# Optimization experiments

Hardware: AMD Instinct MI355X
Metric: run time of the kernel (lower is better)

## Reference

```python
import jax, jax.numpy as jnp
import numpy as np

B, S, D, H = 2, 2048, 512, 8
DH = D // H  # depth per head = 64
MAX_SEQ = 2048


def setup_inputs() -> dict:
    key = jax.random.key(0)
    ks = jax.random.split(key, 12)
    sc = 1.0 / np.sqrt(D)
    inp = {
        "v": jax.random.normal(ks[0], (B, S, D), jnp.float32),
        "k": jax.random.normal(ks[1], (B, S, D), jnp.float32),
        "q": jax.random.normal(ks[2], (B, S, D), jnp.float32),
        # causal look-ahead mask: 1.0 where attention is disallowed (j > i)
        "mask": jnp.triu(jnp.ones((S, S), jnp.float32), k=1)[None, None, :, :],
        "Wq": jax.random.normal(ks[3], (D, D), jnp.float32) * sc,
        "bq": jnp.zeros((D,), jnp.float32),
        "Wk": jax.random.normal(ks[4], (D, D), jnp.float32) * sc,
        "bk": jnp.zeros((D,), jnp.float32),
        "Wv": jax.random.normal(ks[5], (D, D), jnp.float32) * sc,
        "bv": jnp.zeros((D,), jnp.float32),
        "Wo": jax.random.normal(ks[6], (D, D), jnp.float32) * sc,
        "bo": jnp.zeros((D,), jnp.float32),
        # relative position embedding table [max_seq, depth]
        "E": jax.random.normal(ks[7], (MAX_SEQ, DH), jnp.float32) * 0.02,
    }
    return inp


def reference(v, k, q, mask, Wq, bq, Wk, bk, Wv, bv, Wo, bo, E):
    b, s, d = q.shape
    split = lambda x: x.reshape(b, s, H, DH).transpose(0, 2, 1, 3)  # [b,h,s,dh]
    qh = split(q @ Wq + bq)
    kh = split(k @ Wk + bk)
    vh = split(v @ Wv + bv)

    # QK^T logits [b,h,lq,lk]
    logits = jnp.einsum("bhqd,bhkd->bhqk", qh, kh)

    # relative position bias (Music Transformer skewing trick)
    Eq = E[max(MAX_SEQ - s, 0):, :]          # left embedding slice [s, dh]
    m = Eq.shape[0]
    QE = jnp.einsum("bhld,md->bhlm", qh, Eq)  # [b,h,s,m]
    # keep entries where col >= m-1-row (qe masking)
    rows = jnp.arange(s)[:, None]
    cols = jnp.arange(m)[None, :]
    QE = QE * (cols >= (m - 1 - rows)).astype(QE.dtype)
    # skew: pad one zero column on the left, reshape, drop first row
    padded = jnp.pad(QE, ((0, 0), (0, 0), (0, 0), (1, 0)))  # [b,h,s,m+1]
    Srel = padded.reshape(b, H, m + 1, s)[:, :, 1:, :]       # [b,h,m,s]
    # here len_q == len_k == s, so Srel is [b,h,s,s] with no extra pad/slice

    logits = (logits + Srel) / jnp.sqrt(jnp.float32(DH))
    logits = logits + mask * -1e9
    attn = jax.nn.softmax(logits, axis=-1)
    out = jnp.einsum("bhqk,bhkd->bhqd", attn, vh)
    out = out.transpose(0, 2, 1, 3).reshape(b, s, d)
    return out @ Wo + bo, attn
```

## Files before the change

### kernel.cpp

```cpp
#include <hip/hip_runtime.h>

typedef __bf16 bf16x8 __attribute__((ext_vector_type(8)));
typedef float f32x4 __attribute__((ext_vector_type(4)));

#define MFMA(a, b, c) __builtin_amdgcn_mfma_f32_16x16x32_bf16((a), (b), (c), 0, 0, 0)

__global__ __launch_bounds__(256)
void prep_kernel(const float* __restrict__ Wq, const float* __restrict__ Wk,
                 const float* __restrict__ Wv, const float* __restrict__ Wo,
                 const float* __restrict__ E,
                 __bf16* __restrict__ WT, __bf16* __restrict__ Ebf)
{
    __shared__ float tl[32][33];
    const int bx = blockIdx.x, t = threadIdx.x;
    if (bx < 1024) {
        const int wi = bx >> 8, tile = bx & 255;
        const float* W = wi == 0 ? Wq : wi == 1 ? Wk : wi == 2 ? Wv : Wo;
        __bf16* dst = WT + (size_t)wi * 512 * 512;
        const int k0 = (tile >> 4) << 5, n0 = (tile & 15) << 5;
        const int tx = t & 31, ty = t >> 5;
        #pragma unroll
        for (int i = 0; i < 4; ++i) {
            int r = ty + i * 8;
            tl[r][tx] = W[(size_t)(k0 + r) * 512 + n0 + tx];
        }
        __syncthreads();
        #pragma unroll
        for (int i = 0; i < 4; ++i) {
            int r = ty + i * 8;
            dst[(size_t)(n0 + r) * 512 + k0 + tx] = (__bf16)tl[tx][r];
        }
    } else {
        int idx = (bx - 1024) * 256 + t;
        for (int i = idx; i < 2048 * 64; i += 8 * 256)
            Ebf[i] = (__bf16)E[i];
    }
}

__global__ __launch_bounds__(256, 3)
void proj_kernel(const float* __restrict__ xq, const float* __restrict__ xk,
                 const float* __restrict__ xv, const __bf16* __restrict__ WT,
                 const float* __restrict__ bq, const float* __restrict__ bk,
                 const float* __restrict__ bv,
                 __bf16* __restrict__ outQ, __bf16* __restrict__ outK,
                 __bf16* __restrict__ outV)
{
    __shared__ __bf16 As[128][72];
    __shared__ __bf16 Bs[64][72];
    const int t = threadIdx.x;
    const int z = blockIdx.y;
    const float* x = z == 0 ? xq : z == 1 ? xk : xv;
    const float* bias = z == 0 ? bq : z == 1 ? bk : bv;
    const __bf16* Wt = WT + (size_t)z * (512 * 512);
    __bf16* outp = z == 0 ? outQ : z == 1 ? outK : outV;

    const int bx = blockIdx.x;
    const int m0 = (bx >> 3) << 7;
    const int n0 = (bx & 7) << 6;
    const int w = t >> 6, lane = t & 63, quad = lane >> 4, l16 = lane & 15;

    const int ar = t >> 1, ac = (t & 1) << 5;
    const int br = t >> 2, bc = (t & 3) << 4;

    float4 xr[8];
    int4 wr0, wr1;
    {
        const float4* xs = (const float4*)(x + (size_t)(m0 + ar) * 512 + ac);
        #pragma unroll
        for (int j = 0; j < 8; ++j) xr[j] = xs[j];
        const int4* wsrc = (const int4*)(Wt + (size_t)(n0 + br) * 512 + bc);
        wr0 = wsrc[0]; wr1 = wsrc[1];
    }

    f32x4 acc[2][4];
    #pragma unroll
    for (int rb = 0; rb < 2; ++rb)
        #pragma unroll
        for (int nt = 0; nt < 4; ++nt) acc[rb][nt] = (f32x4)0.f;

    for (int k0 = 0; k0 < 512; k0 += 64) {
        __syncthreads();
        {
            __bf16 tb[32];
            #pragma unroll
            for (int j = 0; j < 8; ++j) {
                tb[j * 4 + 0] = (__bf16)xr[j].x;
                tb[j * 4 + 1] = (__bf16)xr[j].y;
                tb[j * 4 + 2] = (__bf16)xr[j].z;
                tb[j * 4 + 3] = (__bf16)xr[j].w;
            }
            *(int4*)&As[ar][ac]      = ((int4*)tb)[0];
            *(int4*)&As[ar][ac + 8]  = ((int4*)tb)[1];
            *(int4*)&As[ar][ac + 16] = ((int4*)tb)[2];
            *(int4*)&As[ar][ac + 24] = ((int4*)tb)[3];
            *(int4*)&Bs[br][bc]     = wr0;
            *(int4*)&Bs[br][bc + 8] = wr1;
        }
        __syncthreads();
        if (k0 + 64 < 512) {
            const float4* xs = (const float4*)(x + (size_t)(m0 + ar) * 512 + k0 + 64 + ac);
            #pragma unroll
            for (int j = 0; j < 8; ++j) xr[j] = xs[j];
            const int4* wsrc = (const int4*)(Wt + (size_t)(n0 + br) * 512 + k0 + 64 + bc);
            wr0 = wsrc[0]; wr1 = wsrc[1];
        }
        bf16x8 bf[8];
        #pragma unroll
        for (int nt = 0; nt < 4; ++nt) {
            bf[nt * 2]     = *(const bf16x8*)&Bs[nt * 16 + l16][quad * 8];
            bf[nt * 2 + 1] = *(const bf16x8*)&Bs[nt * 16 + l16][32 + quad * 8];
        }
        #pragma unroll
        for (int rb = 0; rb < 2; ++rb) {
            bf16x8 a0 = *(const bf16x8*)&As[w * 32 + rb * 16 + l16][quad * 8];
            bf16x8 a1 = *(const bf16x8*)&As[w * 32 + rb * 16 + l16][32 + quad * 8];
            #pragma unroll
            for (int nt = 0; nt < 4; ++nt) {
                acc[rb][nt] = MFMA(a0, bf[nt * 2], acc[rb][nt]);
                acc[rb][nt] = MFMA(a1, bf[nt * 2 + 1], acc[rb][nt]);
            }
        }
    }
    #pragma unroll
    for (int rb = 0; rb < 2; ++rb) {
        #pragma unroll
        for (int nt = 0; nt < 4; ++nt) {
            const int n = n0 + nt * 16 + l16;
            const float bb = bias[n];
            const int h = n >> 6, dh = n & 63;
            #pragma unroll
            for (int i = 0; i < 4; ++i) {
                const int m = m0 + w * 32 + rb * 16 + quad * 4 + i;
                const int b = m >> 11, s = m & 2047;
                outp[(((size_t)(b * 8 + h) * 2048 + s) << 6) + dh] = (__bf16)(acc[rb][nt][i] + bb);
            }
        }
    }
}

__global__ __launch_bounds__(256, 3)
void attn_kernel(const __bf16* __restrict__ Qh, const __bf16* __restrict__ Kh,
                 const __bf16* __restrict__ Vh, const __bf16* __restrict__ Eb,
                 __bf16* __restrict__ Pout, float* __restrict__ attn,
                 __bf16* __restrict__ ctx)
{
    __shared__ __bf16 SA[64][72];
    __shared__ __bf16 SB[64][72];
    __shared__ __bf16 SC[128][72];
    __shared__ float linv_s[64];

    const int t = threadIdx.x;
    const int bx = blockIdx.x;
    const int tt = bx & 31;
    const int bh = ((bx & 255) >> 5) + ((bx >> 8) << 3);
    const int q0 = (bx < 256 ? (31 - tt) : tt) << 6;
    const int w = t >> 6, lane = t & 63, quad = lane >> 4, l16 = lane & 15;
    const int qw = w << 4;

    const __bf16* Qg = Qh + (size_t)bh * (2048 * 64);
    const __bf16* Kg = Kh + (size_t)bh * (2048 * 64);
    const __bf16* Vg = Vh + (size_t)bh * (2048 * 64);
    __bf16* Pg = Pout + (size_t)bh * (2048 * 2048);
    float* attng = attn + (size_t)bh * (2048 * 2048);

    const int sr = t >> 2, sc = (t & 3) << 4;
    const int er = t >> 1, ec = (t & 1) << 5;

    {
        const int4* src = (const int4*)(Qg + (size_t)(q0 + sr) * 64 + sc);
        int4 v0 = src[0], v1 = src[1];
        *(int4*)&SA[sr][sc]     = v0;
        *(int4*)&SA[sr][sc + 8] = v1;
    }
    __syncthreads();
    const bf16x8 qa0 = *(const bf16x8*)&SA[qw + l16][quad * 8];
    const bf16x8 qa1 = *(const bf16x8*)&SA[qw + l16][32 + quad * 8];
    __syncthreads();

    __bf16 (* const Ps)[72] = SA;

    const int nkt = (q0 >> 6) + 1;
    const float csc = 0.125f * 1.44269504f;

    float lsum[4] = {0.f, 0.f, 0.f, 0.f};

    int4 kreg0, kreg1, ereg0, ereg1, ereg2, ereg3;
    {
        const int4* ks = (const int4*)(Kg + (size_t)sr * 64 + sc);
        kreg0 = ks[0]; kreg1 = ks[1];
        int e = 1984 - q0 + er; if (e > 2047) e = 2047;
        const int4* es = (const int4*)(Eb + (size_t)e * 64 + ec);
        ereg0 = es[0]; ereg1 = es[1]; ereg2 = es[2]; ereg3 = es[3];
    }

    for (int kt = 0; kt < nkt; ++kt) {
        const int k0 = kt << 6;
        if (kt > 0) {
            int4 p0 = *(const int4*)&Ps[sr][sc];
            int4 p1 = *(const int4*)&Ps[sr][sc + 8];
            __bf16* dst = Pg + (size_t)(q0 + sr) * 2048 + (k0 - 64) + sc;
            *(int4*)dst       = p0;
            *(int4*)(dst + 8) = p1;
        }
        *(int4*)&SB[sr][sc]     = kreg0;
        *(int4*)&SB[sr][sc + 8] = kreg1;
        *(int4*)&SC[er][ec]      = ereg0;
        *(int4*)&SC[er][ec + 8]  = ereg1;
        *(int4*)&SC[er][ec + 16] = ereg2;
        *(int4*)&SC[er][ec + 24] = ereg3;
        __syncthreads();

        if (kt + 1 < nkt) {
            const int k0n = (kt + 1) << 6;
            const int4* ks = (const int4*)(Kg + (size_t)(k0n + sr) * 64 + sc);
            kreg0 = ks[0]; kreg1 = ks[1];
            int e = 1984 - q0 + k0n + er; if (e > 2047) e = 2047;
            const int4* es = (const int4*)(Eb + (size_t)e * 64 + ec);
            ereg0 = es[0]; ereg1 = es[1]; ereg2 = es[2]; ereg3 = es[3];
        }

        f32x4 aqk[4];
        #pragma unroll
        for (int nt = 0; nt < 4; ++nt) {
            aqk[nt] = (f32x4)0.f;
            bf16x8 b0 = *(const bf16x8*)&SB[nt * 16 + l16][quad * 8];
            bf16x8 b1 = *(const bf16x8*)&SB[nt * 16 + l16][32 + quad * 8];
            aqk[nt] = MFMA(qa0, b0, aqk[nt]);
            aqk[nt] = MFMA(qa1, b1, aqk[nt]);
        }
        f32x4 aqe[5];
        #pragma unroll
        for (int jj = 0; jj < 5; ++jj) {
            aqe[jj] = (f32x4)0.f;
            const int ebr = 48 - qw + jj * 16 + l16;
            bf16x8 b0 = *(const bf16x8*)&SC[ebr][quad * 8];
            bf16x8 b1 = *(const bf16x8*)&SC[ebr][32 + quad * 8];
            aqe[jj] = MFMA(qa0, b0, aqe[jj]);
            aqe[jj] = MFMA(qa1, b1, aqe[jj]);
        }

        #pragma unroll
        for (int i = 0; i < 4; ++i) {
            const int d  = quad * 4 + i;
            const int ql = qw + d;
            const int qq = q0 + ql;
            const int sp = (l16 + 15 - d) & 15;
            const bool hi = l16 > d;
            #pragma unroll
            for (int nt = 0; nt < 4; ++nt) {
                float g0 = __shfl(aqe[nt][i], sp, 16);
                float g1 = __shfl(aqe[nt + 1][i], sp, 16);
                float qe = hi ? g1 : g0;
                float ev = (k0 + nt * 16 + l16 <= qq)
                         ? exp2f((aqk[nt][i] + qe) * csc) : 0.f;
                lsum[i] += ev;
                Ps[ql][nt * 16 + l16] = (__bf16)ev;
            }
        }
        __syncthreads();
    }
    {
        int4 p0 = *(const int4*)&Ps[sr][sc];
        int4 p1 = *(const int4*)&Ps[sr][sc + 8];
        __bf16* dst = Pg + (size_t)(q0 + sr) * 2048 + ((nkt - 1) << 6) + sc;
        *(int4*)dst       = p0;
        *(int4*)(dst + 8) = p1;
    }
    {
        #pragma unroll
        for (int i = 0; i < 4; ++i) {
            float v = lsum[i];
            #pragma unroll
            for (int m = 1; m < 16; m <<= 1) v += __shfl_xor(v, m, 16);
            if (l16 == 0) linv_s[qw + quad * 4 + i] = 1.0f / v;
        }
    }
    __syncthreads();

    const float li = linv_s[qw + l16];
    float linvr[4];
    #pragma unroll
    for (int i = 0; i < 4; ++i) linvr[i] = linv_s[qw + quad * 4 + i];

    f32x4 acc_o[4];
    #pragma unroll
    for (int i = 0; i < 4; ++i) acc_o[i] = (f32x4)0.f;

    int4 vreg0, vreg1;
    {
        const int4* vs = (const int4*)(Vg + (size_t)sr * 64 + sc);
        vreg0 = vs[0]; vreg1 = vs[1];
    }

    for (int kt = 0; kt < nkt; ++kt) {
        const int k0 = kt << 6;
        __syncthreads();
        {
            __bf16 tmp[16];
            *(int4*)&tmp[0] = vreg0; *(int4*)&tmp[8] = vreg1;
            #pragma unroll
            for (int j = 0; j < 16; ++j) {
                const int dh = sc + j;
                SB[dh][sr ^ (((dh >> 4) & 1) << 3)] = tmp[j];
            }
        }
        __syncthreads();
        if (kt + 1 < nkt) {
            const int4* vs = (const int4*)(Vg + (size_t)(((kt + 1) << 6) + sr) * 64 + sc);
            vreg0 = vs[0]; vreg1 = vs[1];
        }

        const __bf16* prow = Pg + (size_t)(q0 + qw + l16) * 2048 + k0 + quad * 8;
        int4 praw0 = *(const int4*)prow;
        int4 praw1 = *(const int4*)(prow + 32);
        bf16x8 pa0 = *(bf16x8*)&praw0;
        bf16x8 pa1 = *(bf16x8*)&praw1;

        #pragma unroll
        for (int dt = 0; dt < 4; ++dt) {
            const int xr = (dt & 1) << 3;
            bf16x8 vb0 = *(const bf16x8*)&SB[dt * 16 + l16][(quad * 8) ^ xr];
            bf16x8 vb1 = *(const bf16x8*)&SB[dt * 16 + l16][32 + ((quad * 8) ^ xr)];
            acc_o[dt] = MFMA(pa0, vb0, acc_o[dt]);
            acc_o[dt] = MFMA(pa1, vb1, acc_o[dt]);
        }

        {
            float* arow = attng + (size_t)(q0 + qw + l16) * 2048 + k0 + quad * 8;
            float4 o;
            o.x = (float)pa0[0] * li; o.y = (float)pa0[1] * li;
            o.z = (float)pa0[2] * li; o.w = (float)pa0[3] * li;
            *(float4*)arow = o;
            o.x = (float)pa0[4] * li; o.y = (float)pa0[5] * li;
            o.z = (float)pa0[6] * li; o.w = (float)pa0[7] * li;
            *(float4*)(arow + 4) = o;
            o.x = (float)pa1[0] * li; o.y = (float)pa1[1] * li;
            o.z = (float)pa1[2] * li; o.w = (float)pa1[3] * li;
            *(float4*)(arow + 32) = o;
            o.x = (float)pa1[4] * li; o.y = (float)pa1[5] * li;
            o.z = (float)pa1[6] * li; o.w = (float)pa1[7] * li;
            *(float4*)(arow + 36) = o;
        }
    }

    {
        const int b = bh >> 3, h = bh & 7;
        #pragma unroll
        for (int dt = 0; dt < 4; ++dt) {
            #pragma unroll
            for (int i = 0; i < 4; ++i) {
                const int qq = q0 + qw + quad * 4 + i;
                const int d = dt * 16 + l16;
                ctx[((size_t)(b * 2048 + qq) * 512) + h * 64 + d] =
                    (__bf16)(acc_o[dt][i] * linvr[i]);
            }
        }
    }
    {
        const int kend = q0 + 64;
        const int zc = 2048 - kend;
        if (zc > 0) {
            const int zq = zc >> 2;
            const float4 z4 = make_float4(0.f, 0.f, 0.f, 0.f);
            for (int idx = t; idx < 64 * zq; idx += 256) {
                int r = idx / zq, c = idx - r * zq;
                *(float4*)&attng[(size_t)(q0 + r) * 2048 + kend + c * 4] = z4;
            }
        }
    }
}

__global__ __launch_bounds__(256, 2)
void outproj_kernel(const __bf16* __restrict__ ctx, const __bf16* __restrict__ WoT,
                    const float* __restrict__ bo, float* __restrict__ out)
{
    __shared__ __bf16 As[64][72];
    __shared__ __bf16 Bs[64][72];
    const int t = threadIdx.x;
    const int bx = blockIdx.x;
    const int m0 = (bx >> 3) << 6;
    const int n0 = (bx & 7) << 6;
    const int w = t >> 6, lane = t & 63, quad = lane >> 4, l16 = lane & 15;
    const int r = t >> 2, c0 = (t & 3) << 4;

    int4 ar0, ar1, br0, br1;
    {
        const int4* asrc = (const int4*)(ctx + (size_t)(m0 + r) * 512 + c0);
        ar0 = asrc[0]; ar1 = asrc[1];
        const int4* bsrc = (const int4*)(WoT + (size_t)(n0 + r) * 512 + c0);
        br0 = bsrc[0]; br1 = bsrc[1];
    }

    f32x4 acc[4];
    #pragma unroll
    for (int i = 0; i < 4; ++i) acc[i] = (f32x4)0.f;

    for (int k0 = 0; k0 < 512; k0 += 64) {
        __syncthreads();
        *(int4*)&As[r][c0]     = ar0;
        *(int4*)&As[r][c0 + 8] = ar1;
        *(int4*)&Bs[r][c0]     = br0;
        *(int4*)&Bs[r][c0 + 8] = br1;
        __syncthreads();
        if (k0 + 64 < 512) {
            const int4* asrc = (const int4*)(ctx + (size_t)(m0 + r) * 512 + k0 + 64 + c0);
            ar0 = asrc[0]; ar1 = asrc[1];
            const int4* bsrc = (const int4*)(WoT + (size_t)(n0 + r) * 512 + k0 + 64 + c0);
            br0 = bsrc[0]; br1 = bsrc[1];
        }
        bf16x8 a0 = *(const bf16x8*)&As[(w << 4) + l16][quad * 8];
        bf16x8 a1 = *(const bf16x8*)&As[(w << 4) + l16][32 + quad * 8];
        #pragma unroll
        for (int nt = 0; nt < 4; ++nt) {
            bf16x8 b0 = *(const bf16x8*)&Bs[nt * 16 + l16][quad * 8];
            bf16x8 b1 = *(const bf16x8*)&Bs[nt * 16 + l16][32 + quad * 8];
            acc[nt] = MFMA(a0, b0, acc[nt]);
            acc[nt] = MFMA(a1, b1, acc[nt]);
        }
    }
    #pragma unroll
    for (int nt = 0; nt < 4; ++nt) {
        const int n = n0 + nt * 16 + l16;
        const float bb = bo[n];
        #pragma unroll
        for (int i = 0; i < 4; ++i) {
            const int m = m0 + (w << 4) + quad * 4 + i;
            out[(size_t)m * 512 + n] = acc[nt][i] + bb;
        }
    }
}

extern "C" void kernel_launch(void* const* d_in, const int* in_sizes, int n_in,
                              void* d_out, int out_size, void* d_ws, size_t ws_size,
                              hipStream_t stream) {
    const float* v  = (const float*)d_in[0];
    const float* k  = (const float*)d_in[1];
    const float* q  = (const float*)d_in[2];
    const float* Wq = (const float*)d_in[4];
    const float* bq = (const float*)d_in[5];
    const float* Wk = (const float*)d_in[6];
    const float* bk = (const float*)d_in[7];
    const float* Wv = (const float*)d_in[8];
    const float* bv = (const float*)d_in[9];
    const float* Wo = (const float*)d_in[10];
    const float* bo = (const float*)d_in[11];
    const float* E  = (const float*)d_in[12];

    float* out  = (float*)d_out;
    float* attn = out + (size_t)2 * 2048 * 512;

    char* ws = (char*)d_ws;
    __bf16* WT   = (__bf16*)ws;
    __bf16* Ebf  = (__bf16*)(ws + (size_t)(4 * 512 * 512) * 2);
    __bf16* Qh   = Ebf + (size_t)2048 * 64;
    __bf16* Kh   = Qh + (size_t)16 * 2048 * 64;
    __bf16* Vh   = Kh + (size_t)16 * 2048 * 64;
    __bf16* ctx  = Vh + (size_t)16 * 2048 * 64;
    __bf16* Pout = ctx + (size_t)16 * 2048 * 64;

    prep_kernel<<<1032, 256, 0, stream>>>(Wq, Wk, Wv, Wo, E, WT, Ebf);
    proj_kernel<<<dim3(256, 3), 256, 0, stream>>>(q, k, v, WT, bq, bk, bv, Qh, Kh, Vh);
    attn_kernel<<<512, 256, 0, stream>>>(Qh, Kh, Vh, Ebf, Pout, attn, ctx);
    outproj_kernel<<<512, 256, 0, stream>>>(ctx, WT + (size_t)3 * 512 * 512, bo, out);
}
```

Before: 454.8 us.

## Drop LDS staging in attention; read K/E/V^T directly from global memory

```diff
diff --git a/kernel.cpp b/kernel.cpp
--- a/kernel.cpp
+++ b/kernel.cpp
@@ -43,7 +43,7 @@
                  const float* __restrict__ bq, const float* __restrict__ bk,
                  const float* __restrict__ bv,
                  __bf16* __restrict__ outQ, __bf16* __restrict__ outK,
-                 __bf16* __restrict__ outV)
+                 __bf16* __restrict__ outVT)
 {
     __shared__ __bf16 As[128][72];
     __shared__ __bf16 Bs[64][72];
@@ -52,7 +52,6 @@
     const float* x = z == 0 ? xq : z == 1 ? xk : xv;
     const float* bias = z == 0 ? bq : z == 1 ? bk : bv;
     const __bf16* Wt = WT + (size_t)z * (512 * 512);
-    __bf16* outp = z == 0 ? outQ : z == 1 ? outK : outV;
 
     const int bx = blockIdx.x;
     const int m0 = (bx >> 3) << 7;
@@ -132,21 +131,24 @@
             for (int i = 0; i < 4; ++i) {
                 const int m = m0 + w * 32 + rb * 16 + quad * 4 + i;
                 const int b = m >> 11, s = m & 2047;
-                outp[(((size_t)(b * 8 + h) * 2048 + s) << 6) + dh] = (__bf16)(acc[rb][nt][i] + bb);
-            }
-        }
-    }
-}
-
-__global__ __launch_bounds__(256, 3)
+                const __bf16 val = (__bf16)(acc[rb][nt][i] + bb);
+                if (z == 2) {
+                    outVT[((size_t)((b * 8 + h) * 64 + dh)) * 2048 + s] = val;
+                } else {
+                    __bf16* outp = z == 0 ? outQ : outK;
+                    outp[(((size_t)(b * 8 + h) * 2048 + s) << 6) + dh] = val;
+                }
+            }
+        }
+    }
+}
+
+__global__ __launch_bounds__(256, 4)
 void attn_kernel(const __bf16* __restrict__ Qh, const __bf16* __restrict__ Kh,
-                 const __bf16* __restrict__ Vh, const __bf16* __restrict__ Eb,
+                 const __bf16* __restrict__ VhT, const __bf16* __restrict__ Eb,
                  __bf16* __restrict__ Pout, float* __restrict__ attn,
                  __bf16* __restrict__ ctx)
 {
-    __shared__ __bf16 SA[64][72];
-    __shared__ __bf16 SB[64][72];
-    __shared__ __bf16 SC[128][72];
     __shared__ float linv_s[64];
 
     const int t = threadIdx.x;
@@ -159,93 +161,48 @@
 
     const __bf16* Qg = Qh + (size_t)bh * (2048 * 64);
     const __bf16* Kg = Kh + (size_t)bh * (2048 * 64);
-    const __bf16* Vg = Vh + (size_t)bh * (2048 * 64);
+    const __bf16* Vt = VhT + (size_t)bh * (64 * 2048);
     __bf16* Pg = Pout + (size_t)bh * (2048 * 2048);
     float* attng = attn + (size_t)bh * (2048 * 2048);
 
-    const int sr = t >> 2, sc = (t & 3) << 4;
-    const int er = t >> 1, ec = (t & 1) << 5;
-
-    {
-        const int4* src = (const int4*)(Qg + (size_t)(q0 + sr) * 64 + sc);
-        int4 v0 = src[0], v1 = src[1];
-        *(int4*)&SA[sr][sc]     = v0;
-        *(int4*)&SA[sr][sc + 8] = v1;
-    }
-    __syncthreads();
-    const bf16x8 qa0 = *(const bf16x8*)&SA[qw + l16][quad * 8];
-    const bf16x8 qa1 = *(const bf16x8*)&SA[qw + l16][32 + quad * 8];
-    __syncthreads();
-
-    __bf16 (* const Ps)[72] = SA;
-
     const int nkt = (q0 >> 6) + 1;
     const float csc = 0.125f * 1.44269504f;
 
+    const int qrow = q0 + qw + l16;
+    const bf16x8 qa0 = *(const bf16x8*)(Qg + (size_t)qrow * 64 + quad * 8);
+    const bf16x8 qa1 = *(const bf16x8*)(Qg + (size_t)qrow * 64 + 32 + quad * 8);
+
     float lsum[4] = {0.f, 0.f, 0.f, 0.f};
-
-    int4 kreg0, kreg1, ereg0, ereg1, ereg2, ereg3;
-    {
-        const int4* ks = (const int4*)(Kg + (size_t)sr * 64 + sc);
-        kreg0 = ks[0]; kreg1 = ks[1];
-        int e = 1984 - q0 + er; if (e > 2047) e = 2047;
-        const int4* es = (const int4*)(Eb + (size_t)e * 64 + ec);
-        ereg0 = es[0]; ereg1 = es[1]; ereg2 = es[2]; ereg3 = es[3];
-    }
 
     for (int kt = 0; kt < nkt; ++kt) {
         const int k0 = kt << 6;
-        if (kt > 0) {
-            int4 p0 = *(const int4*)&Ps[sr][sc];
-            int4 p1 = *(const int4*)&Ps[sr][sc + 8];
-            __bf16* dst = Pg + (size_t)(q0 + sr) * 2048 + (k0 - 64) + sc;
-            *(int4*)dst       = p0;
-            *(int4*)(dst + 8) = p1;
-        }
-        *(int4*)&SB[sr][sc]     = kreg0;
-        *(int4*)&SB[sr][sc + 8] = kreg1;
-        *(int4*)&SC[er][ec]      = ereg0;
-        *(int4*)&SC[er][ec + 8]  = ereg1;
-        *(int4*)&SC[er][ec + 16] = ereg2;
-        *(int4*)&SC[er][ec + 24] = ereg3;
-        __syncthreads();
-
-        if (kt + 1 < nkt) {
-            const int k0n = (kt + 1) << 6;
-            const int4* ks = (const int4*)(Kg + (size_t)(k0n + sr) * 64 + sc);
-            kreg0 = ks[0]; kreg1 = ks[1];
-            int e = 1984 - q0 + k0n + er; if (e > 2047) e = 2047;
-            const int4* es = (const int4*)(Eb + (size_t)e * 64 + ec);
-            ereg0 = es[0]; ereg1 = es[1]; ereg2 = es[2]; ereg3 = es[3];
-        }
-
         f32x4 aqk[4];
         #pragma unroll
         for (int nt = 0; nt < 4; ++nt) {
-            aqk[nt] = (f32x4)0.f;
-            bf16x8 b0 = *(const bf16x8*)&SB[nt * 16 + l16][quad * 8];
-            bf16x8 b1 = *(const bf16x8*)&SB[nt * 16 + l16][32 + quad * 8];
-            aqk[nt] = MFMA(qa0, b0, aqk[nt]);
+            const __bf16* kp = Kg + (size_t)(k0 + nt * 16 + l16) * 64 + quad * 8;
+            bf16x8 b0 = *(const bf16x8*)kp;
+            bf16x8 b1 = *(const bf16x8*)(kp + 32);
+            aqk[nt] = MFMA(qa0, b0, (f32x4)0.f);
             aqk[nt] = MFMA(qa1, b1, aqk[nt]);
         }
         f32x4 aqe[5];
         #pragma unroll
         for (int jj = 0; jj < 5; ++jj) {
-            aqe[jj] = (f32x4)0.f;
-            const int ebr = 48 - qw + jj * 16 + l16;
-            bf16x8 b0 = *(const bf16x8*)&SC[ebr][quad * 8];
-            bf16x8 b1 = *(const bf16x8*)&SC[ebr][32 + quad * 8];
-            aqe[jj] = MFMA(qa0, b0, aqe[jj]);
+            int e = 1984 - q0 + k0 + 48 - qw + jj * 16 + l16;
+            if (e > 2047) e = 2047;
+            const __bf16* ep = Eb + (size_t)e * 64 + quad * 8;
+            bf16x8 b0 = *(const bf16x8*)ep;
+            bf16x8 b1 = *(const bf16x8*)(ep + 32);
+            aqe[jj] = MFMA(qa0, b0, (f32x4)0.f);
             aqe[jj] = MFMA(qa1, b1, aqe[jj]);
         }
-
         #pragma unroll
         for (int i = 0; i < 4; ++i) {
             const int d  = quad * 4 + i;
-            const int ql = qw + d;
-            const int qq = q0 + ql;
+            const int qq = q0 + qw + d;
             const int sp = (l16 + 15 - d) & 15;
             const bool hi = l16 > d;
+            __bf16* prow = Pg + (size_t)qq * 2048 + k0 + l16;
             #pragma unroll
             for (int nt = 0; nt < 4; ++nt) {
                 float g0 = __shfl(aqe[nt][i], sp, 16);
@@ -254,28 +211,19 @@
                 float ev = (k0 + nt * 16 + l16 <= qq)
                          ? exp2f((aqk[nt][i] + qe) * csc) : 0.f;
                 lsum[i] += ev;
-                Ps[ql][nt * 16 + l16] = (__bf16)ev;
-            }
-        }
-        __syncthreads();
-    }
-    {
-        int4 p0 = *(const int4*)&Ps[sr][sc];
-        int4 p1 = *(const int4*)&Ps[sr][sc + 8];
-        __bf16* dst = Pg + (size_t)(q0 + sr) * 2048 + ((nkt - 1) << 6) + sc;
-        *(int4*)dst       = p0;
-        *(int4*)(dst + 8) = p1;
-    }
-    {
-        #pragma unroll
-        for (int i = 0; i < 4; ++i) {
-            float v = lsum[i];
-            #pragma unroll
-            for (int m = 1; m < 16; m <<= 1) v += __shfl_xor(v, m, 16);
-            if (l16 == 0) linv_s[qw + quad * 4 + i] = 1.0f / v;
-        }
+                prow[nt * 16] = (__bf16)ev;
+            }
+        }
+    }
+    #pragma unroll
+    for (int i = 0; i < 4; ++i) {
+        float v = lsum[i];
+        #pragma unroll
+        for (int m = 1; m < 16; m <<= 1) v += __shfl_xor(v, m, 16);
+        if (l16 == 0) linv_s[qw + quad * 4 + i] = 1.0f / v;
     }
     __syncthreads();
+    __threadfence();
 
     const float li = linv_s[qw + l16];
     float linvr[4];
@@ -286,31 +234,9 @@
     #pragma unroll
     for (int i = 0; i < 4; ++i) acc_o[i] = (f32x4)0.f;
 
-    int4 vreg0, vreg1;
-    {
-        const int4* vs = (const int4*)(Vg + (size_t)sr * 64 + sc);
-        vreg0 = vs[0]; vreg1 = vs[1];
-    }
-
     for (int kt = 0; kt < nkt; ++kt) {
         const int k0 = kt << 6;
-        __syncthreads();
-        {
-            __bf16 tmp[16];
-            *(int4*)&tmp[0] = vreg0; *(int4*)&tmp[8] = vreg1;
-            #pragma unroll
-            for (int j = 0; j < 16; ++j) {
-                const int dh = sc + j;
-                SB[dh][sr ^ (((dh >> 4) & 1) << 3)] = tmp[j];
-            }
-        }
-        __syncthreads();
-        if (kt + 1 < nkt) {
-            const int4* vs = (const int4*)(Vg + (size_t)(((kt + 1) << 6) + sr) * 64 + sc);
-            vreg0 = vs[0]; vreg1 = vs[1];
-        }
-
-        const __bf16* prow = Pg + (size_t)(q0 + qw + l16) * 2048 + k0 + quad * 8;
+        const __bf16* prow = Pg + (size_t)qrow * 2048 + k0 + quad * 8;
         int4 praw0 = *(const int4*)prow;
         int4 praw1 = *(const int4*)(prow + 32);
         bf16x8 pa0 = *(bf16x8*)&praw0;
@@ -318,29 +244,27 @@
 
         #pragma unroll
         for (int dt = 0; dt < 4; ++dt) {
-            const int xr = (dt & 1) << 3;
-            bf16x8 vb0 = *(const bf16x8*)&SB[dt * 16 + l16][(quad * 8) ^ xr];
-            bf16x8 vb1 = *(const bf16x8*)&SB[dt * 16 + l16][32 + ((quad * 8) ^ xr)];
+            const __bf16* vp = Vt + (size_t)(dt * 16 + l16) * 2048 + k0 + quad * 8;
+            bf16x8 vb0 = *(const bf16x8*)vp;
+            bf16x8 vb1 = *(const bf16x8*)(vp + 32);
             acc_o[dt] = MFMA(pa0, vb0, acc_o[dt]);
             acc_o[dt] = MFMA(pa1, vb1, acc_o[dt]);
         }
 
-        {
-            float* arow = attng + (size_t)(q0 + qw + l16) * 2048 + k0 + quad * 8;
-            float4 o;
-            o.x = (float)pa0[0] * li; o.y = (float)pa0[1] * li;
-            o.z = (float)pa0[2] * li; o.w = (float)pa0[3] * li;
-            *(float4*)arow = o;
-            o.x = (float)pa0[4] * li; o.y = (float)pa0[5] * li;
-            o.z = (float)pa0[6] * li; o.w = (float)pa0[7] * li;
-            *(float4*)(arow + 4) = o;
-            o.x = (float)pa1[0] * li; o.y = (float)pa1[1] * li;
-            o.z = (float)pa1[2] * li; o.w = (float)pa1[3] * li;
-            *(float4*)(arow + 32) = o;
-            o.x = (float)pa1[4] * li; o.y = (float)pa1[5] * li;
-            o.z = (float)pa1[6] * li; o.w = (float)pa1[7] * li;
-            *(float4*)(arow + 36) = o;
-        }
+        float* arow = attng + (size_t)qrow * 2048 + k0 + quad * 8;
+        f32x4 o;
+        o[0] = (float)pa0[0] * li; o[1] = (float)pa0[1] * li;
+        o[2] = (float)pa0[2] * li; o[3] = (float)pa0[3] * li;
+        __builtin_nontemporal_store(o, (f32x4*)arow);
+        o[0] = (float)pa0[4] * li; o[1] = (float)pa0[5] * li;
+        o[2] = (float)pa0[6] * li; o[3] = (float)pa0[7] * li;
+        __builtin_nontemporal_store(o, (f32x4*)(arow + 4));
+        o[0] = (float)pa1[0] * li; o[1] = (float)pa1[1] * li;
+        o[2] = (float)pa1[2] * li; o[3] = (float)pa1[3] * li;
+        __builtin_nontemporal_store(o, (f32x4*)(arow + 32));
+        o[0] = (float)pa1[4] * li; o[1] = (float)pa1[5] * li;
+        o[2] = (float)pa1[6] * li; o[3] = (float)pa1[7] * li;
+        __builtin_nontemporal_store(o, (f32x4*)(arow + 36));
     }
 
     {
@@ -361,10 +285,11 @@
         const int zc = 2048 - kend;
         if (zc > 0) {
             const int zq = zc >> 2;
-            const float4 z4 = make_float4(0.f, 0.f, 0.f, 0.f);
+            const f32x4 z4 = (f32x4)0.f;
             for (int idx = t; idx < 64 * zq; idx += 256) {
                 int r = idx / zq, c = idx - r * zq;
-                *(float4*)&attng[(size_t)(q0 + r) * 2048 + kend + c * 4] = z4;
+                __builtin_nontemporal_store(
+                    z4, (f32x4*)&attng[(size_t)(q0 + r) * 2048 + kend + c * 4]);
             }
         }
     }
@@ -454,12 +379,12 @@
     __bf16* Ebf  = (__bf16*)(ws + (size_t)(4 * 512 * 512) * 2);
     __bf16* Qh   = Ebf + (size_t)2048 * 64;
     __bf16* Kh   = Qh + (size_t)16 * 2048 * 64;
-    __bf16* Vh   = Kh + (size_t)16 * 2048 * 64;
-    __bf16* ctx  = Vh + (size_t)16 * 2048 * 64;
+    __bf16* VhT  = Kh + (size_t)16 * 2048 * 64;
+    __bf16* ctx  = VhT + (size_t)16 * 2048 * 64;
     __bf16* Pout = ctx + (size_t)16 * 2048 * 64;
 
     prep_kernel<<<1032, 256, 0, stream>>>(Wq, Wk, Wv, Wo, E, WT, Ebf);
-    proj_kernel<<<dim3(256, 3), 256, 0, stream>>>(q, k, v, WT, bq, bk, bv, Qh, Kh, Vh);
-    attn_kernel<<<512, 256, 0, stream>>>(Qh, Kh, Vh, Ebf, Pout, attn, ctx);
+    proj_kernel<<<dim3(256, 3), 256, 0, stream>>>(q, k, v, WT, bq, bk, bv, Qh, Kh, VhT);
+    attn_kernel<<<512, 256, 0, stream>>>(Qh, Kh, VhT, Ebf, Pout, attn, ctx);
     outproj_kernel<<<512, 256, 0, stream>>>(ctx, WT + (size_t)3 * 512 * 512, bo, out);
 }
```

Result: slower. 609.8 us (+34.1%).
